# Kernel tuning notes

Measured on AMD Instinct MI355X. Metric: run time of the kernel, lower is better.

Reference implementation:

```python
import jax, jax.numpy as jnp
import numpy as np

B, W, M = 16, 32, 512
NH, HALF, K, H = 64, 32, 8, 8
LK = W // 2               # long-conv kernel size
LOUT = W - 2 * (LK - 1)   # = 2 (dilated valid conv output length)
NSP = 10                  # n_spatial (hardcoded in module)
GC1_IN = (1 + LOUT) * K   # 24


def setup_inputs() -> dict:
    key = jax.random.key(0)
    ks = jax.random.split(key, 23)
    def n(k, shp, s=0.1):
        return jax.random.normal(k, shp, jnp.float32) * s
    return dict(
        x=jax.random.normal(ks[0], (B, W, M), jnp.float32),
        adj=jax.random.uniform(ks[1], (M, M), jnp.float32) / M,  # row-normalized-ish dense adj
        Wih=n(ks[2], (NH, 1)), Whh=n(ks[3], (NH, NH)),
        bih=n(ks[4], (NH,)), bhh=n(ks[5], (NH,)),
        W1=n(ks[6], (HALF, NH)), W2=n(ks[7], (HALF, NH)), b1=n(ks[8], (HALF,)),
        V=n(ks[9], (HALF,)), bv=n(ks[10], (1,)),
        Wb=n(ks[11], (M, M)), wb=n(ks[12], (1,)),
        conv_w=n(ks[13], (K, 1, W)), conv_b=n(ks[14], (K,)),
        convl_w=n(ks[15], (K, 1, LK)), convl_b=n(ks[16], (K,)),
        gc1_w=n(ks[17], (GC1_IN, NH)), gc1_b=n(ks[18], (NH,)),
        gc2_w=n(ks[19], (NH, NSP)), gc2_b=n(ks[20], (NSP,)),
        out_w=n(ks[21], (H, NSP + NH)), out_b=n(ks[22], (H,)),
    )


def reference(x, adj, Wih, Whh, bih, bhh, W1, W2, b1, V, bv, Wb, wb,
              conv_w, conv_b, convl_w, convl_b, gc1_w, gc1_b, gc2_w, gc2_b,
              out_w, out_b):
    b = x.shape[0]
    # [b, w, m] -> per-node sequences [b*m, w]
    seq = jnp.transpose(x, (0, 2, 1)).reshape(b * M, W)

    # vanilla tanh RNN, input_size=1 (batched over all b*m series)
    inp = seq[:, :, None] * Wih[:, 0] + (bih + bhh)          # [b*m, w, nh]
    def step(h, it):
        return jnp.tanh(it + h @ Whh.T), None
    h0 = jnp.zeros((b * M, NH), x.dtype)
    last_hid, _ = jax.lax.scan(step, h0, jnp.swapaxes(inp, 0, 1))
    last_hid = last_hid.reshape(b, M, NH)                    # out_temporal

    # pairwise additive attention: a[b,i,j] = V . elu(W1 h_j + W2 h_i + b1) + bv
    e1 = last_hid @ W1.T                                     # [b, m, half] (j role)
    e2 = last_hid @ W2.T                                     # [b, m, half] (i role)
    a = jax.nn.elu(e2[:, :, None, :] + e1[:, None, :, :] + b1)  # [b,m,m,half]
    a_mx = a @ V + bv                                        # [b, m, m]
    # F.normalize(p=2, dim=1)
    norm = jnp.sqrt(jnp.sum(a_mx * a_mx, axis=1, keepdims=True))
    a_mx = a_mx / jnp.maximum(norm, 1e-12)

    # per-node short conv (kernel == window -> out len 1) as a single matmul
    r_short = seq @ conv_w[:, 0, :].T + conv_b               # [b*m, k]
    # per-node dilated long conv, batched over all b*m series
    r_long = jax.lax.conv_general_dilated(
        seq[:, None, :], convl_w, window_strides=(1,), padding='VALID',
        rhs_dilation=(2,), dimension_numbers=('NCW', 'OIW', 'NCW'))
    r_long = r_long + convl_b[None, :, None]                 # [b*m, k, LOUT]
    r = jnp.concatenate([r_short[:, :, None], r_long], axis=-1)  # [b*m, k, 1+LOUT]
    r = jax.nn.relu(r.reshape(b, M, GC1_IN))

    # gated mix of static normalized adj and learned attention adj
    c = jax.nn.sigmoid(a_mx @ Wb + wb)
    adj_mix = adj[None] * c + a_mx * (1.0 - c)               # [b, m, m]

    # two dense graph conv layers: relu(adj @ (h @ W) + b)
    h1 = jax.nn.relu(adj_mix @ (r @ gc1_w) + gc1_b)          # [b, m, nh]
    out_spatial = jax.nn.relu(adj_mix @ (h1 @ gc2_w) + gc2_b)  # [b, m, nsp]

    feat = jnp.concatenate([out_spatial, last_hid], axis=-1)  # [b, m, nsp+nh]
    out = feat @ out_w.T + out_b                              # [b, m, h]
    return jnp.transpose(out, (0, 2, 1))                      # [b, h, m]
```

## Files before the change

### kernel.cpp

```cpp
#include <hip/hip_runtime.h>


typedef __attribute__((ext_vector_type(8))) short bf16x8;
typedef __attribute__((ext_vector_type(4))) float f32x4;
#define MFMA16 __builtin_amdgcn_mfma_f32_16x16x32_bf16

__device__ __forceinline__ unsigned short f2bf(float f) {
    unsigned u = __float_as_uint(f);
    u += 0x7fff + ((u >> 16) & 1);
    return (unsigned short)(u >> 16);
}
__device__ __forceinline__ float bf2f(unsigned short h) {
    return __uint_as_float(((unsigned)h) << 16);
}
__device__ __forceinline__ float fast_tanh(float x) {
    float e = __expf(2.f * x);
    return 1.f - 2.f / (e + 1.f);
}

__global__ __launch_bounds__(256) void fused1_kernel(
    const float* __restrict__ x, const float* __restrict__ Wih,
    const float* __restrict__ Whh, const float* __restrict__ bih,
    const float* __restrict__ bhh, const float* __restrict__ W1,
    const float* __restrict__ W2, float* __restrict__ lh,
    float* __restrict__ e1, float* __restrict__ e2,
    const float* __restrict__ conv_w, const float* __restrict__ conv_b,
    const float* __restrict__ convl_w, const float* __restrict__ convl_b,
    const float* __restrict__ gc1_w, unsigned short* __restrict__ rgT,
    const float* __restrict__ Wb, unsigned short* __restrict__ WbT,
    float* __restrict__ nrmss)
{
    __shared__ __align__(16) char smem[12160];
    int blk = blockIdx.x, t = threadIdx.x;

    if (blk < 256) {
        int wid = t >> 6, lane = t & 63;
        int rowblk = blk * 32;
        int b = rowblk >> 9, mb = rowblk & 511;
        float* xs = (float*)smem;
        unsigned short* hs = (unsigned short*)(smem + 4096);
        float* rrs = (float*)(smem + 8704);

        for (int u = t; u < 1024; u += 256) {
            int tt = u >> 5, c = u & 31;
            xs[tt * 32 + c] = x[(b * 32 + tt) * 512 + mb + c];
        }
        for (int u = t; u < 2304; u += 256) hs[u] = 0;
        __syncthreads();

        if (wid < 2) {
            int l15 = lane & 15, quad = lane >> 4;
            int row0 = rowblk + wid * 16;
            unsigned short* hw0 = hs + wid * 1152;

            bf16x8 afr[4][2];
#pragma unroll
            for (int mt = 0; mt < 4; ++mt)
#pragma unroll
                for (int hf = 0; hf < 2; ++hf) {
                    const float* src = Whh + (16 * mt + l15) * 64 + 32 * hf + quad * 8;
                    union { bf16x8 v; unsigned short u[8]; } tmp;
#pragma unroll
                    for (int j = 0; j < 8; ++j) tmp.u[j] = f2bf(src[j]);
                    afr[mt][hf] = tmp.v;
                }
            bf16x8 wfr[2][2][2];
#pragma unroll
            for (int e = 0; e < 2; ++e)
#pragma unroll
                for (int nt = 0; nt < 2; ++nt)
#pragma unroll
                    for (int kf = 0; kf < 2; ++kf) {
                        const float* Wsrc = (e ? W2 : W1);
                        const float* src = Wsrc + (16 * nt + l15) * 64 + 32 * kf + quad * 8;
                        union { bf16x8 v; unsigned short u[8]; } tmp;
#pragma unroll
                        for (int j = 0; j < 8; ++j) tmp.u[j] = f2bf(src[j]);
                        wfr[e][nt][kf] = tmp.v;
                    }
            float wihv[4][4], bsv[4][4];
#pragma unroll
            for (int mt = 0; mt < 4; ++mt)
#pragma unroll
                for (int r = 0; r < 4; ++r) {
                    int n = 16 * mt + quad * 4 + r;
                    wihv[mt][r] = Wih[n];
                    bsv[mt][r]  = bih[n] + bhh[n];
                }

            float th[4][4];
            for (int tstep = 0; tstep < 32; ++tstep) {
                bf16x8 b0 = *(bf16x8*)(hw0 + l15 * 72 + quad * 8);
                bf16x8 b1 = *(bf16x8*)(hw0 + l15 * 72 + 32 + quad * 8);
                float xt = xs[tstep * 32 + wid * 16 + l15];
                f32x4 acc[4];
#pragma unroll
                for (int mt = 0; mt < 4; ++mt) {
                    f32x4 z = {0.f, 0.f, 0.f, 0.f};
                    acc[mt] = MFMA16(afr[mt][0], b0, z, 0, 0, 0);
                    acc[mt] = MFMA16(afr[mt][1], b1, acc[mt], 0, 0, 0);
                }
#pragma unroll
                for (int mt = 0; mt < 4; ++mt) {
                    ushort4 hwv;
#pragma unroll
                    for (int r = 0; r < 4; ++r)
                        th[mt][r] = fast_tanh(acc[mt][r] + xt * wihv[mt][r] + bsv[mt][r]);
                    hwv.x = f2bf(th[mt][0]); hwv.y = f2bf(th[mt][1]);
                    hwv.z = f2bf(th[mt][2]); hwv.w = f2bf(th[mt][3]);
                    *(ushort4*)(hw0 + l15 * 72 + 16 * mt + quad * 4) = hwv;
                }
            }
#pragma unroll
            for (int mt = 0; mt < 4; ++mt)
                *(float4*)(lh + (row0 + l15) * 64 + 16 * mt + quad * 4) =
                    make_float4(th[mt][0], th[mt][1], th[mt][2], th[mt][3]);

            bf16x8 a0 = *(bf16x8*)(hw0 + l15 * 72 + quad * 8);
            bf16x8 a1 = *(bf16x8*)(hw0 + l15 * 72 + 32 + quad * 8);
#pragma unroll
            for (int e = 0; e < 2; ++e) {
                float* dst = e ? e2 : e1;
#pragma unroll
                for (int nt = 0; nt < 2; ++nt) {
                    f32x4 z = {0.f, 0.f, 0.f, 0.f};
                    f32x4 ee = MFMA16(a0, wfr[e][nt][0], z, 0, 0, 0);
                    ee = MFMA16(a1, wfr[e][nt][1], ee, 0, 0, 0);
#pragma unroll
                    for (int r = 0; r < 4; ++r)
                        dst[(row0 + quad * 4 + r) * 32 + 16 * nt + l15] = ee[r];
                }
            }
        } else {
            int wid2 = wid - 2;
#pragma unroll
            for (int rep = 0; rep < 2; ++rep) {
                int task = rep * 64 + lane;
                int rl = wid2 * 16 + (task >> 3);
                int k  = task & 7;
                float s = conv_b[k];
                for (int w = 0; w < 32; ++w) s += xs[w * 32 + rl] * conv_w[k * 32 + w];
                float l0 = convl_b[k], l1 = l0;
                for (int tt = 0; tt < 16; ++tt) {
                    float wv = convl_w[k * 16 + tt];
                    l0 += xs[(2 * tt) * 32 + rl] * wv;
                    l1 += xs[(2 * tt + 1) * 32 + rl] * wv;
                }
                rrs[rl * 25 + k * 3 + 0] = fmaxf(s, 0.f);
                rrs[rl * 25 + k * 3 + 1] = fmaxf(l0, 0.f);
                rrs[rl * 25 + k * 3 + 2] = fmaxf(l1, 0.f);
            }
            __builtin_amdgcn_wave_barrier();
            int rl = wid2 * 16 + (lane & 15);
            int nb = lane >> 4;
#pragma unroll
            for (int q = 0; q < 16; ++q) {
                int n = nb * 16 + q;
                float acc = 0.f;
#pragma unroll
                for (int c = 0; c < 24; ++c) acc += rrs[rl * 25 + c] * gc1_w[c * 64 + n];
                rgT[b * 32768 + n * 512 + mb + rl] = f2bf(acc);
            }
        }
    } else if (blk < 512) {
        int bid = blk - 256;
        int nb = (bid & 15) * 32, kb = (bid >> 4) * 32;
        float* tile = (float*)smem;
        for (int u = t; u < 1024; u += 256) {
            int r = u >> 5, c = u & 31;
            tile[r * 33 + c] = Wb[(kb + r) * 512 + nb + c];
        }
        __syncthreads();
        for (int u = t; u < 1024; u += 256) {
            int r = u >> 5, c = u & 31;
            WbT[(nb + r) * 512 + kb + c] = f2bf(tile[c * 33 + r]);
        }
    } else {
        nrmss[(blk - 512) * 256 + t] = 0.f;
    }
}

__global__ __launch_bounds__(256) void amx_kernel(
    const float* __restrict__ e1, const float* __restrict__ e2,
    const float* __restrict__ b1p, const float* __restrict__ Vp,
    const float* __restrict__ bvp, unsigned short* __restrict__ amxb,
    float* __restrict__ nrmss)
{
    int bb = blockIdx.z;
    int i0 = blockIdx.y * 64, j0 = blockIdx.x * 64;
    __shared__ float e2s[64][33], e1s[64][33];
    __shared__ float Vs[32];
    __shared__ float red[16][68];
    int t = threadIdx.x;
    for (int u = t; u < 2048; u += 256) {
        int r = u >> 5, c = u & 31;
        e2s[r][c] = e2[(bb * 512 + i0 + r) * 32 + c];
        e1s[r][c] = e1[(bb * 512 + j0 + r) * 32 + c] + b1p[c];
    }
    if (t < 32) Vs[t] = Vp[t];
    __syncthreads();
    int ti = (t >> 4) * 4, tj = (t & 15) * 4;
    float acc[4][4] = {};
#pragma unroll
    for (int h = 0; h < 32; ++h) {
        float vv = Vs[h];
        float xi[4], yj[4], Exi[4], Eyj[4];
#pragma unroll
        for (int p = 0; p < 4; ++p) { xi[p] = e2s[ti + p][h]; Exi[p] = __expf(xi[p]); }
#pragma unroll
        for (int q = 0; q < 4; ++q) { yj[q] = e1s[tj + q][h]; Eyj[q] = __expf(yj[q]); }
#pragma unroll
        for (int p = 0; p < 4; ++p)
#pragma unroll
            for (int q = 0; q < 4; ++q) {
                float v = xi[p] + yj[q];
                float prod = Exi[p] * Eyj[q];
                float el = v > 0.f ? v : prod - 1.f;
                acc[p][q] += vv * el;
            }
    }
    float bv = bvp[0];
    float ss[4] = {0.f, 0.f, 0.f, 0.f};
#pragma unroll
    for (int p = 0; p < 4; ++p) {
        float v0 = acc[p][0] + bv, v1 = acc[p][1] + bv;
        float v2 = acc[p][2] + bv, v3 = acc[p][3] + bv;
        ushort4 o;
        o.x = f2bf(v0); o.y = f2bf(v1); o.z = f2bf(v2); o.w = f2bf(v3);
        *(ushort4*)(amxb + (bb * 512 + i0 + ti + p) * 512 + j0 + tj) = o;
        ss[0] += v0 * v0; ss[1] += v1 * v1; ss[2] += v2 * v2; ss[3] += v3 * v3;
    }
#pragma unroll
    for (int q = 0; q < 4; ++q) red[t >> 4][tj + q] = ss[q];
    __syncthreads();
    if (t < 64) {
        float s = 0.f;
#pragma unroll
        for (int g = 0; g < 16; ++g) s += red[g][t];
        atomicAdd(&nrmss[bb * 512 + j0 + t], s);
    }
}

__global__ __launch_bounds__(256) void gemm_adjmix(
    const unsigned short* __restrict__ amxb, const unsigned short* __restrict__ WbT,
    const float* __restrict__ wbp, const float* __restrict__ adj,
    const float* __restrict__ nrmss, unsigned short* __restrict__ adjmix)
{
    int bb = blockIdx.z;
    int i0 = blockIdx.y * 64, j0 = blockIdx.x * 64;
    __shared__ __align__(16) short As[64 * 72];
    __shared__ __align__(16) short Bs[64 * 72];
    __shared__ float rn[512];
    int t = threadIdx.x, w = t >> 6, lane = t & 63;
    int l15 = lane & 15, quad = lane >> 4;
    for (int u = t; u < 512; u += 256)
        rn[u] = 1.f / fmaxf(sqrtf(nrmss[bb * 512 + u]), 1e-12f);
    const unsigned short* Ag = amxb + bb * 262144;
    f32x4 acc[4] = {};
    for (int kk = 1; kk <= 8; ++kk) {
        int k0 = (j0 + 64 * kk) & 511;
        __syncthreads();
#pragma unroll
        for (int u0 = 0; u0 < 2; ++u0) {
            int u = t + u0 * 256;
            int i = u >> 3, o = u & 7;
            *(int4*)(Bs + i * 72 + o * 8) =
                *(const int4*)(WbT + (j0 + i) * 512 + k0 + o * 8);
            union { int4 v; unsigned short us[8]; } ur;
            ur.v = *(const int4*)(Ag + (i0 + i) * 512 + k0 + o * 8);
            union { int4 v; unsigned short us[8]; } ow;
#pragma unroll
            for (int c = 0; c < 8; ++c)
                ow.us[c] = f2bf(bf2f(ur.us[c]) * rn[k0 + o * 8 + c]);
            *(int4*)(As + i * 72 + o * 8) = ow.v;
        }
        __syncthreads();
        bf16x8 a0 = *(bf16x8*)(As + (16 * w + l15) * 72 + quad * 8);
        bf16x8 a1 = *(bf16x8*)(As + (16 * w + l15) * 72 + 32 + quad * 8);
#pragma unroll
        for (int nt = 0; nt < 4; ++nt) {
            bf16x8 b0 = *(bf16x8*)(Bs + (16 * nt + l15) * 72 + quad * 8);
            bf16x8 b1 = *(bf16x8*)(Bs + (16 * nt + l15) * 72 + 32 + quad * 8);
            acc[nt] = MFMA16(a0, b0, acc[nt], 0, 0, 0);
            acc[nt] = MFMA16(a1, b1, acc[nt], 0, 0, 0);
        }
    }
    float wb = wbp[0];
#pragma unroll
    for (int nt = 0; nt < 4; ++nt)
#pragma unroll
    for (int r = 0; r < 4; ++r) {
        int il = 16 * w + quad * 4 + r;
        int jl = 16 * nt + l15;
        int i = i0 + il, j = j0 + jl;
        float s  = acc[nt][r] + wb;
        float cv = 1.f / (1.f + __expf(-s));
        float am = bf2f((unsigned short)As[il * 72 + jl]);
        float ad = adj[i * 512 + j];
        adjmix[(bb * 512 + i) * 512 + j] = f2bf(ad * cv + am * (1.f - cv));
    }
}

__global__ __launch_bounds__(256) void gemm_h1(
    const unsigned short* __restrict__ adjmix, const unsigned short* __restrict__ rgT,
    const float* __restrict__ gc1_b, const float* __restrict__ gc2_w,
    float* __restrict__ h1g)
{
    int bb = blockIdx.y;
    int i0 = blockIdx.x * 32;
    __shared__ __align__(16) short As[32 * 72];
    __shared__ __align__(16) short Bs[64 * 72];
    __shared__ float h1s[32][72];
    int t = threadIdx.x, w = t >> 6, lane = t & 63;
    int l15 = lane & 15, quad = lane >> 4;
    int rt = w & 1, ntb = (w >> 1) * 2;
    const unsigned short* Ag = adjmix + bb * 262144;
    const unsigned short* Bg = rgT + bb * 32768;
    f32x4 acc[2] = {};
    for (int k0 = 0; k0 < 512; k0 += 64) {
        __syncthreads();
        {
            int i = t >> 3, o = t & 7;
            *(int4*)(As + i * 72 + o * 8) =
                *(const int4*)(Ag + (i0 + i) * 512 + k0 + o * 8);
        }
#pragma unroll
        for (int u0 = 0; u0 < 2; ++u0) {
            int u = t + u0 * 256;
            int i = u >> 3, o = u & 7;
            *(int4*)(Bs + i * 72 + o * 8) =
                *(const int4*)(Bg + i * 512 + k0 + o * 8);
        }
        __syncthreads();
        bf16x8 a0 = *(bf16x8*)(As + (16 * rt + l15) * 72 + quad * 8);
        bf16x8 a1 = *(bf16x8*)(As + (16 * rt + l15) * 72 + 32 + quad * 8);
#pragma unroll
        for (int q = 0; q < 2; ++q) {
            int nt = ntb + q;
            bf16x8 b0 = *(bf16x8*)(Bs + (16 * nt + l15) * 72 + quad * 8);
            bf16x8 b1 = *(bf16x8*)(Bs + (16 * nt + l15) * 72 + 32 + quad * 8);
            acc[q] = MFMA16(a0, b0, acc[q], 0, 0, 0);
            acc[q] = MFMA16(a1, b1, acc[q], 0, 0, 0);
        }
    }
#pragma unroll
    for (int q = 0; q < 2; ++q)
#pragma unroll
    for (int r = 0; r < 4; ++r) {
        int il = 16 * rt + quad * 4 + r;
        int j = 16 * (ntb + q) + l15;
        h1s[il][j] = fmaxf(acc[q][r] + gc1_b[j], 0.f);
    }
    __syncthreads();
    for (int u = t; u < 320; u += 256) {
        int row = u / 10, ns = u - row * 10;
        float a2 = 0.f;
#pragma unroll
        for (int j = 0; j < 64; ++j) a2 += h1s[row][j] * gc2_w[j * 10 + ns];
        h1g[(bb * 512 + i0 + row) * 10 + ns] = a2;
    }
}

__global__ __launch_bounds__(256) void ospout_kernel(
    const unsigned short* __restrict__ adjmix, const float* __restrict__ h1g,
    const float* __restrict__ gc2_b, const float* __restrict__ lh,
    const float* __restrict__ out_w, const float* __restrict__ out_b,
    float* __restrict__ out)
{
    int r0 = blockIdx.x * 16;
    int bb = r0 >> 9;
    int wid = threadIdx.x >> 6, lane = threadIdx.x & 63;
    __shared__ float Bsm[10][512];
    __shared__ float ow[8][80];
    __shared__ float ob[8], g2b[10];
    for (int u = threadIdx.x; u < 5120; u += 256) {
        int k = u / 10, ns = u - k * 10;
        Bsm[ns][k] = h1g[bb * 5120 + u];
    }
    if (threadIdx.x < 8)  ob[threadIdx.x]  = out_b[threadIdx.x];
    if (threadIdx.x < 10) g2b[threadIdx.x] = gc2_b[threadIdx.x];
    for (int u = threadIdx.x; u < 592; u += 256) {
        int hh = u / 74, c = u - hh * 74;
        ow[hh][c] = out_w[u];
    }
    __syncthreads();
#pragma unroll
    for (int half = 0; half < 4; ++half) {
        int row = r0 + half * 4 + wid, m = row & 511;
        const unsigned short* Ar = adjmix + row * 512;
        float a[8];
#pragma unroll
        for (int q = 0; q < 8; ++q) a[q] = bf2f(Ar[lane + 64 * q]);
        float os[10];
#pragma unroll
        for (int ns = 0; ns < 10; ++ns) {
            float s = 0.f;
#pragma unroll
            for (int q = 0; q < 8; ++q) s += a[q] * Bsm[ns][lane + 64 * q];
#pragma unroll
            for (int off = 32; off; off >>= 1) s += __shfl_xor(s, off);
            os[ns] = fmaxf(s + g2b[ns], 0.f);
        }
        float lv = lh[row * 64 + lane];
#pragma unroll
        for (int hh = 0; hh < 8; ++hh) {
            float t1 = lv * ow[hh][10 + lane];
#pragma unroll
            for (int off = 32; off; off >>= 1) t1 += __shfl_xor(t1, off);
            if (lane == hh) {
                float acc = ob[hh] + t1;
#pragma unroll
                for (int ns = 0; ns < 10; ++ns) acc += os[ns] * ow[hh][ns];
                out[bb * 4096 + hh * 512 + m] = acc;
            }
        }
    }
}

extern "C" void kernel_launch(void* const* d_in, const int* in_sizes, int n_in,
                              void* d_out, int out_size, void* d_ws, size_t ws_size,
                              hipStream_t stream)
{
    const float* x       = (const float*)d_in[0];
    const float* adj     = (const float*)d_in[1];
    const float* Wih     = (const float*)d_in[2];
    const float* Whh     = (const float*)d_in[3];
    const float* bih     = (const float*)d_in[4];
    const float* bhh     = (const float*)d_in[5];
    const float* W1      = (const float*)d_in[6];
    const float* W2      = (const float*)d_in[7];
    const float* b1      = (const float*)d_in[8];
    const float* V       = (const float*)d_in[9];
    const float* bv      = (const float*)d_in[10];
    const float* Wb      = (const float*)d_in[11];
    const float* wb      = (const float*)d_in[12];
    const float* conv_w  = (const float*)d_in[13];
    const float* conv_b  = (const float*)d_in[14];
    const float* convl_w = (const float*)d_in[15];
    const float* convl_b = (const float*)d_in[16];
    const float* gc1_w   = (const float*)d_in[17];
    const float* gc1_b   = (const float*)d_in[18];
    const float* gc2_w   = (const float*)d_in[19];
    const float* gc2_b   = (const float*)d_in[20];
    const float* out_w   = (const float*)d_in[21];
    const float* out_b   = (const float*)d_in[22];

    float* ws    = (float*)d_ws;
    float* lh    = ws;
    float* e1    = lh + 524288;
    float* e2    = e1 + 262144;
    float* nrmss = e2 + 262144;
    float* h1g   = nrmss + 8192;
    unsigned short* amxb    = (unsigned short*)(h1g + 81920);
    unsigned short* adjmixb = amxb + 4194304;
    unsigned short* WbT     = adjmixb + 4194304;
    unsigned short* rgT     = WbT + 262144;

    fused1_kernel<<<544, 256, 0, stream>>>(
        x, Wih, Whh, bih, bhh, W1, W2, lh, e1, e2,
        conv_w, conv_b, convl_w, convl_b, gc1_w, rgT, Wb, WbT, nrmss);
    amx_kernel<<<dim3(8, 8, 16), 256, 0, stream>>>(e1, e2, b1, V, bv,
                                                   amxb, nrmss);
    gemm_adjmix<<<dim3(8, 8, 16), 256, 0, stream>>>(amxb, WbT, wb, adj,
                                                    nrmss, adjmixb);
    gemm_h1<<<dim3(16, 16), 256, 0, stream>>>(adjmixb, rgT, gc1_b, gc2_w, h1g);
    ospout_kernel<<<512, 256, 0, stream>>>(adjmixb, h1g, gc2_b, lh,
                                           out_w, out_b, (float*)d_out);
}
```

Before: 207.1 us.

## Merge five kernels into one persistent kernel with global atomic barriers

Replaces the chain of five kernel launches with a single 512-block persistent kernel whose phases (RNN/conv, attention scores, adjacency-mix GEMM, first graph conv, output) are separated by a software grid barrier built on an atomic counter and spin-wait. The aim is to remove launch gaps and tail effects between stages. In exchange, the kernel relies on all 512 blocks being co-resident (launch_bounds 256,2 with enlarged shared memory), adds barrier spin overhead, and fixes the phase work into a static loop over 1024 tiles. A memset of the barrier counter is added before the launch.

```diff
diff --git a/kernel.cpp b/kernel.cpp
--- a/kernel.cpp
+++ b/kernel.cpp
@@ -18,7 +18,21 @@
     return 1.f - 2.f / (e + 1.f);
 }
 
-__global__ __launch_bounds__(256) void fused1_kernel(
+__device__ __forceinline__ void gbar(unsigned* bar, unsigned phase) {
+    __syncthreads();
+    if (threadIdx.x == 0) {
+        __threadfence();
+        atomicAdd(bar, 1u);
+        unsigned tgt = phase * 512u;
+        while (__hip_atomic_load(bar, __ATOMIC_ACQUIRE,
+                                 __HIP_MEMORY_SCOPE_AGENT) < tgt)
+            __builtin_amdgcn_s_sleep(2);
+        __threadfence();
+    }
+    __syncthreads();
+}
+
+__global__ __launch_bounds__(256, 2) void mega_kernel(
     const float* __restrict__ x, const float* __restrict__ Wih,
     const float* __restrict__ Whh, const float* __restrict__ bih,
     const float* __restrict__ bhh, const float* __restrict__ W1,
@@ -28,9 +42,18 @@
     const float* __restrict__ convl_w, const float* __restrict__ convl_b,
     const float* __restrict__ gc1_w, unsigned short* __restrict__ rgT,
     const float* __restrict__ Wb, unsigned short* __restrict__ WbT,
-    float* __restrict__ nrmss)
+    float* __restrict__ nrmss,
+    const float* __restrict__ b1p, const float* __restrict__ Vp,
+    const float* __restrict__ bvp, unsigned short* __restrict__ amxb,
+    const float* __restrict__ wbp, const float* __restrict__ adj,
+    unsigned short* __restrict__ adjmix,
+    const float* __restrict__ gc1_b, const float* __restrict__ gc2_w,
+    float* __restrict__ h1g,
+    const float* __restrict__ gc2_b,
+    const float* __restrict__ out_w, const float* __restrict__ out_b,
+    float* __restrict__ out, unsigned* __restrict__ bar)
 {
-    __shared__ __align__(16) char smem[12160];
+    __shared__ __align__(16) char smem[23296];
     int blk = blockIdx.x, t = threadIdx.x;
 
     if (blk < 256) {
@@ -162,10 +185,11 @@
                 rgT[b * 32768 + n * 512 + mb + rl] = f2bf(acc);
             }
         }
-    } else if (blk < 512) {
+    } else {
         int bid = blk - 256;
         int nb = (bid & 15) * 32, kb = (bid >> 4) * 32;
         float* tile = (float*)smem;
+        if (bid < 32) nrmss[bid * 256 + t] = 0.f;
         for (int u = t; u < 1024; u += 256) {
             int r = u >> 5, c = u & 31;
             tile[r * 33 + c] = Wb[(kb + r) * 512 + nb + c];
@@ -175,243 +199,234 @@
             int r = u >> 5, c = u & 31;
             WbT[(nb + r) * 512 + kb + c] = f2bf(tile[c * 33 + r]);
         }
-    } else {
-        nrmss[(blk - 512) * 256 + t] = 0.f;
-    }
-}
-
-__global__ __launch_bounds__(256) void amx_kernel(
-    const float* __restrict__ e1, const float* __restrict__ e2,
-    const float* __restrict__ b1p, const float* __restrict__ Vp,
-    const float* __restrict__ bvp, unsigned short* __restrict__ amxb,
-    float* __restrict__ nrmss)
-{
-    int bb = blockIdx.z;
-    int i0 = blockIdx.y * 64, j0 = blockIdx.x * 64;
-    __shared__ float e2s[64][33], e1s[64][33];
-    __shared__ float Vs[32];
-    __shared__ float red[16][68];
-    int t = threadIdx.x;
-    for (int u = t; u < 2048; u += 256) {
-        int r = u >> 5, c = u & 31;
-        e2s[r][c] = e2[(bb * 512 + i0 + r) * 32 + c];
-        e1s[r][c] = e1[(bb * 512 + j0 + r) * 32 + c] + b1p[c];
-    }
-    if (t < 32) Vs[t] = Vp[t];
-    __syncthreads();
-    int ti = (t >> 4) * 4, tj = (t & 15) * 4;
-    float acc[4][4] = {};
-#pragma unroll
-    for (int h = 0; h < 32; ++h) {
-        float vv = Vs[h];
-        float xi[4], yj[4], Exi[4], Eyj[4];
-#pragma unroll
-        for (int p = 0; p < 4; ++p) { xi[p] = e2s[ti + p][h]; Exi[p] = __expf(xi[p]); }
-#pragma unroll
-        for (int q = 0; q < 4; ++q) { yj[q] = e1s[tj + q][h]; Eyj[q] = __expf(yj[q]); }
-#pragma unroll
-        for (int p = 0; p < 4; ++p)
-#pragma unroll
-            for (int q = 0; q < 4; ++q) {
-                float v = xi[p] + yj[q];
-                float prod = Exi[p] * Eyj[q];
-                float el = v > 0.f ? v : prod - 1.f;
-                acc[p][q] += vv * el;
-            }
-    }
-    float bv = bvp[0];
-    float ss[4] = {0.f, 0.f, 0.f, 0.f};
-#pragma unroll
-    for (int p = 0; p < 4; ++p) {
-        float v0 = acc[p][0] + bv, v1 = acc[p][1] + bv;
-        float v2 = acc[p][2] + bv, v3 = acc[p][3] + bv;
-        ushort4 o;
-        o.x = f2bf(v0); o.y = f2bf(v1); o.z = f2bf(v2); o.w = f2bf(v3);
-        *(ushort4*)(amxb + (bb * 512 + i0 + ti + p) * 512 + j0 + tj) = o;
-        ss[0] += v0 * v0; ss[1] += v1 * v1; ss[2] += v2 * v2; ss[3] += v3 * v3;
-    }
-#pragma unroll
-    for (int q = 0; q < 4; ++q) red[t >> 4][tj + q] = ss[q];
-    __syncthreads();
-    if (t < 64) {
-        float s = 0.f;
-#pragma unroll
-        for (int g = 0; g < 16; ++g) s += red[g][t];
-        atomicAdd(&nrmss[bb * 512 + j0 + t], s);
-    }
-}
-
-__global__ __launch_bounds__(256) void gemm_adjmix(
-    const unsigned short* __restrict__ amxb, const unsigned short* __restrict__ WbT,
-    const float* __restrict__ wbp, const float* __restrict__ adj,
-    const float* __restrict__ nrmss, unsigned short* __restrict__ adjmix)
-{
-    int bb = blockIdx.z;
-    int i0 = blockIdx.y * 64, j0 = blockIdx.x * 64;
-    __shared__ __align__(16) short As[64 * 72];
-    __shared__ __align__(16) short Bs[64 * 72];
-    __shared__ float rn[512];
-    int t = threadIdx.x, w = t >> 6, lane = t & 63;
-    int l15 = lane & 15, quad = lane >> 4;
-    for (int u = t; u < 512; u += 256)
-        rn[u] = 1.f / fmaxf(sqrtf(nrmss[bb * 512 + u]), 1e-12f);
-    const unsigned short* Ag = amxb + bb * 262144;
-    f32x4 acc[4] = {};
-    for (int kk = 1; kk <= 8; ++kk) {
-        int k0 = (j0 + 64 * kk) & 511;
-        __syncthreads();
-#pragma unroll
-        for (int u0 = 0; u0 < 2; ++u0) {
-            int u = t + u0 * 256;
-            int i = u >> 3, o = u & 7;
-            *(int4*)(Bs + i * 72 + o * 8) =
-                *(const int4*)(WbT + (j0 + i) * 512 + k0 + o * 8);
-            union { int4 v; unsigned short us[8]; } ur;
-            ur.v = *(const int4*)(Ag + (i0 + i) * 512 + k0 + o * 8);
-            union { int4 v; unsigned short us[8]; } ow;
-#pragma unroll
-            for (int c = 0; c < 8; ++c)
-                ow.us[c] = f2bf(bf2f(ur.us[c]) * rn[k0 + o * 8 + c]);
-            *(int4*)(As + i * 72 + o * 8) = ow.v;
-        }
-        __syncthreads();
-        bf16x8 a0 = *(bf16x8*)(As + (16 * w + l15) * 72 + quad * 8);
-        bf16x8 a1 = *(bf16x8*)(As + (16 * w + l15) * 72 + 32 + quad * 8);
-#pragma unroll
-        for (int nt = 0; nt < 4; ++nt) {
-            bf16x8 b0 = *(bf16x8*)(Bs + (16 * nt + l15) * 72 + quad * 8);
-            bf16x8 b1 = *(bf16x8*)(Bs + (16 * nt + l15) * 72 + 32 + quad * 8);
-            acc[nt] = MFMA16(a0, b0, acc[nt], 0, 0, 0);
-            acc[nt] = MFMA16(a1, b1, acc[nt], 0, 0, 0);
-        }
-    }
-    float wb = wbp[0];
-#pragma unroll
-    for (int nt = 0; nt < 4; ++nt)
-#pragma unroll
-    for (int r = 0; r < 4; ++r) {
-        int il = 16 * w + quad * 4 + r;
-        int jl = 16 * nt + l15;
-        int i = i0 + il, j = j0 + jl;
-        float s  = acc[nt][r] + wb;
-        float cv = 1.f / (1.f + __expf(-s));
-        float am = bf2f((unsigned short)As[il * 72 + jl]);
-        float ad = adj[i * 512 + j];
-        adjmix[(bb * 512 + i) * 512 + j] = f2bf(ad * cv + am * (1.f - cv));
-    }
-}
-
-__global__ __launch_bounds__(256) void gemm_h1(
-    const unsigned short* __restrict__ adjmix, const unsigned short* __restrict__ rgT,
-    const float* __restrict__ gc1_b, const float* __restrict__ gc2_w,
-    float* __restrict__ h1g)
-{
-    int bb = blockIdx.y;
-    int i0 = blockIdx.x * 32;
-    __shared__ __align__(16) short As[32 * 72];
-    __shared__ __align__(16) short Bs[64 * 72];
-    __shared__ float h1s[32][72];
-    int t = threadIdx.x, w = t >> 6, lane = t & 63;
-    int l15 = lane & 15, quad = lane >> 4;
-    int rt = w & 1, ntb = (w >> 1) * 2;
-    const unsigned short* Ag = adjmix + bb * 262144;
-    const unsigned short* Bg = rgT + bb * 32768;
-    f32x4 acc[2] = {};
-    for (int k0 = 0; k0 < 512; k0 += 64) {
-        __syncthreads();
-        {
-            int i = t >> 3, o = t & 7;
-            *(int4*)(As + i * 72 + o * 8) =
-                *(const int4*)(Ag + (i0 + i) * 512 + k0 + o * 8);
-        }
-#pragma unroll
-        for (int u0 = 0; u0 < 2; ++u0) {
-            int u = t + u0 * 256;
-            int i = u >> 3, o = u & 7;
-            *(int4*)(Bs + i * 72 + o * 8) =
-                *(const int4*)(Bg + i * 512 + k0 + o * 8);
-        }
-        __syncthreads();
-        bf16x8 a0 = *(bf16x8*)(As + (16 * rt + l15) * 72 + quad * 8);
-        bf16x8 a1 = *(bf16x8*)(As + (16 * rt + l15) * 72 + 32 + quad * 8);
-#pragma unroll
-        for (int q = 0; q < 2; ++q) {
-            int nt = ntb + q;
-            bf16x8 b0 = *(bf16x8*)(Bs + (16 * nt + l15) * 72 + quad * 8);
-            bf16x8 b1 = *(bf16x8*)(Bs + (16 * nt + l15) * 72 + 32 + quad * 8);
-            acc[q] = MFMA16(a0, b0, acc[q], 0, 0, 0);
-            acc[q] = MFMA16(a1, b1, acc[q], 0, 0, 0);
-        }
-    }
-#pragma unroll
-    for (int q = 0; q < 2; ++q)
-#pragma unroll
-    for (int r = 0; r < 4; ++r) {
-        int il = 16 * rt + quad * 4 + r;
-        int j = 16 * (ntb + q) + l15;
-        h1s[il][j] = fmaxf(acc[q][r] + gc1_b[j], 0.f);
-    }
-    __syncthreads();
-    for (int u = t; u < 320; u += 256) {
-        int row = u / 10, ns = u - row * 10;
-        float a2 = 0.f;
-#pragma unroll
-        for (int j = 0; j < 64; ++j) a2 += h1s[row][j] * gc2_w[j * 10 + ns];
-        h1g[(bb * 512 + i0 + row) * 10 + ns] = a2;
-    }
-}
-
-__global__ __launch_bounds__(256) void ospout_kernel(
-    const unsigned short* __restrict__ adjmix, const float* __restrict__ h1g,
-    const float* __restrict__ gc2_b, const float* __restrict__ lh,
-    const float* __restrict__ out_w, const float* __restrict__ out_b,
-    float* __restrict__ out)
-{
-    int r0 = blockIdx.x * 16;
-    int bb = r0 >> 9;
-    int wid = threadIdx.x >> 6, lane = threadIdx.x & 63;
-    __shared__ float Bsm[10][512];
-    __shared__ float ow[8][80];
-    __shared__ float ob[8], g2b[10];
-    for (int u = threadIdx.x; u < 5120; u += 256) {
-        int k = u / 10, ns = u - k * 10;
-        Bsm[ns][k] = h1g[bb * 5120 + u];
-    }
-    if (threadIdx.x < 8)  ob[threadIdx.x]  = out_b[threadIdx.x];
-    if (threadIdx.x < 10) g2b[threadIdx.x] = gc2_b[threadIdx.x];
-    for (int u = threadIdx.x; u < 592; u += 256) {
-        int hh = u / 74, c = u - hh * 74;
-        ow[hh][c] = out_w[u];
-    }
-    __syncthreads();
-#pragma unroll
-    for (int half = 0; half < 4; ++half) {
-        int row = r0 + half * 4 + wid, m = row & 511;
-        const unsigned short* Ar = adjmix + row * 512;
-        float a[8];
-#pragma unroll
-        for (int q = 0; q < 8; ++q) a[q] = bf2f(Ar[lane + 64 * q]);
-        float os[10];
-#pragma unroll
-        for (int ns = 0; ns < 10; ++ns) {
+    }
+
+    gbar(bar, 1);
+
+    for (int tid = blk; tid < 1024; tid += 512) {
+        __syncthreads();
+        int bb = tid >> 6;
+        int i0 = ((tid >> 3) & 7) * 64, j0 = (tid & 7) * 64;
+        float* e2s = (float*)smem;
+        float* e1s = (float*)(smem + 8448);
+        float* Vs  = (float*)(smem + 16896);
+        float* red = (float*)(smem + 17024);
+        for (int u = t; u < 2048; u += 256) {
+            int r = u >> 5, c = u & 31;
+            e2s[r * 33 + c] = e2[(bb * 512 + i0 + r) * 32 + c];
+            e1s[r * 33 + c] = e1[(bb * 512 + j0 + r) * 32 + c] + b1p[c];
+        }
+        if (t < 32) Vs[t] = Vp[t];
+        __syncthreads();
+        int ti = (t >> 4) * 4, tj = (t & 15) * 4;
+        float acc[4][4] = {};
+#pragma unroll
+        for (int h = 0; h < 32; ++h) {
+            float vv = Vs[h];
+            float xi[4], yj[4], Exi[4], Eyj[4];
+#pragma unroll
+            for (int p = 0; p < 4; ++p) { xi[p] = e2s[(ti + p) * 33 + h]; Exi[p] = __expf(xi[p]); }
+#pragma unroll
+            for (int q = 0; q < 4; ++q) { yj[q] = e1s[(tj + q) * 33 + h]; Eyj[q] = __expf(yj[q]); }
+#pragma unroll
+            for (int p = 0; p < 4; ++p)
+#pragma unroll
+                for (int q = 0; q < 4; ++q) {
+                    float v = xi[p] + yj[q];
+                    float prod = Exi[p] * Eyj[q];
+                    float el = v > 0.f ? v : prod - 1.f;
+                    acc[p][q] += vv * el;
+                }
+        }
+        float bv = bvp[0];
+        float ss[4] = {0.f, 0.f, 0.f, 0.f};
+#pragma unroll
+        for (int p = 0; p < 4; ++p) {
+            float v0 = acc[p][0] + bv, v1 = acc[p][1] + bv;
+            float v2 = acc[p][2] + bv, v3 = acc[p][3] + bv;
+            ushort4 o;
+            o.x = f2bf(v0); o.y = f2bf(v1); o.z = f2bf(v2); o.w = f2bf(v3);
+            *(ushort4*)(amxb + (bb * 512 + i0 + ti + p) * 512 + j0 + tj) = o;
+            ss[0] += v0 * v0; ss[1] += v1 * v1; ss[2] += v2 * v2; ss[3] += v3 * v3;
+        }
+#pragma unroll
+        for (int q = 0; q < 4; ++q) red[(t >> 4) * 68 + tj + q] = ss[q];
+        __syncthreads();
+        if (t < 64) {
             float s = 0.f;
 #pragma unroll
-            for (int q = 0; q < 8; ++q) s += a[q] * Bsm[ns][lane + 64 * q];
-#pragma unroll
-            for (int off = 32; off; off >>= 1) s += __shfl_xor(s, off);
-            os[ns] = fmaxf(s + g2b[ns], 0.f);
-        }
-        float lv = lh[row * 64 + lane];
-#pragma unroll
-        for (int hh = 0; hh < 8; ++hh) {
-            float t1 = lv * ow[hh][10 + lane];
-#pragma unroll
-            for (int off = 32; off; off >>= 1) t1 += __shfl_xor(t1, off);
-            if (lane == hh) {
-                float acc = ob[hh] + t1;
-#pragma unroll
-                for (int ns = 0; ns < 10; ++ns) acc += os[ns] * ow[hh][ns];
-                out[bb * 4096 + hh * 512 + m] = acc;
+            for (int g = 0; g < 16; ++g) s += red[g * 68 + t];
+            atomicAdd(&nrmss[bb * 512 + j0 + t], s);
+        }
+    }
+
+    gbar(bar, 2);
+
+    for (int tid = blk; tid < 1024; tid += 512) {
+        __syncthreads();
+        int bb = tid >> 6;
+        int i0 = ((tid >> 3) & 7) * 64, j0 = (tid & 7) * 64;
+        short* As = (short*)smem;
+        short* Bs = (short*)(smem + 9216);
+        float* rn = (float*)(smem + 18432);
+        int w = t >> 6, lane = t & 63;
+        int l15 = lane & 15, quad = lane >> 4;
+        for (int u = t; u < 512; u += 256)
+            rn[u] = 1.f / fmaxf(sqrtf(nrmss[bb * 512 + u]), 1e-12f);
+        const unsigned short* Ag = amxb + bb * 262144;
+        f32x4 acc[4] = {};
+        for (int kk = 1; kk <= 8; ++kk) {
+            int k0 = (j0 + 64 * kk) & 511;
+            __syncthreads();
+#pragma unroll
+            for (int u0 = 0; u0 < 2; ++u0) {
+                int u = t + u0 * 256;
+                int i = u >> 3, o = u & 7;
+                *(int4*)(Bs + i * 72 + o * 8) =
+                    *(const int4*)(WbT + (j0 + i) * 512 + k0 + o * 8);
+                union { int4 v; unsigned short us[8]; } ur;
+                ur.v = *(const int4*)(Ag + (i0 + i) * 512 + k0 + o * 8);
+                union { int4 v; unsigned short us[8]; } ow;
+#pragma unroll
+                for (int c = 0; c < 8; ++c)
+                    ow.us[c] = f2bf(bf2f(ur.us[c]) * rn[k0 + o * 8 + c]);
+                *(int4*)(As + i * 72 + o * 8) = ow.v;
+            }
+            __syncthreads();
+            bf16x8 a0 = *(bf16x8*)(As + (16 * w + l15) * 72 + quad * 8);
+            bf16x8 a1 = *(bf16x8*)(As + (16 * w + l15) * 72 + 32 + quad * 8);
+#pragma unroll
+            for (int nt = 0; nt < 4; ++nt) {
+                bf16x8 b0 = *(bf16x8*)(Bs + (16 * nt + l15) * 72 + quad * 8);
+                bf16x8 b1 = *(bf16x8*)(Bs + (16 * nt + l15) * 72 + 32 + quad * 8);
+                acc[nt] = MFMA16(a0, b0, acc[nt], 0, 0, 0);
+                acc[nt] = MFMA16(a1, b1, acc[nt], 0, 0, 0);
+            }
+        }
+        float wb = wbp[0];
+#pragma unroll
+        for (int nt = 0; nt < 4; ++nt)
+#pragma unroll
+        for (int r = 0; r < 4; ++r) {
+            int il = 16 * w + quad * 4 + r;
+            int jl = 16 * nt + l15;
+            int i = i0 + il, j = j0 + jl;
+            float s  = acc[nt][r] + wb;
+            float cv = 1.f / (1.f + __expf(-s));
+            float am = bf2f((unsigned short)As[il * 72 + jl]);
+            float ad = adj[i * 512 + j];
+            adjmix[(bb * 512 + i) * 512 + j] = f2bf(ad * cv + am * (1.f - cv));
+        }
+    }
+
+    gbar(bar, 3);
+
+    if (blk < 256) {
+        int bb = blk >> 4;
+        int i0 = (blk & 15) * 32;
+        short* As  = (short*)smem;
+        short* Bs  = (short*)(smem + 4608);
+        float* h1s = (float*)(smem + 13824);
+        int w = t >> 6, lane = t & 63;
+        int l15 = lane & 15, quad = lane >> 4;
+        int rt = w & 1, ntb = (w >> 1) * 2;
+        const unsigned short* Ag = adjmix + bb * 262144;
+        const unsigned short* Bg = rgT + bb * 32768;
+        f32x4 acc[2] = {};
+        for (int k0 = 0; k0 < 512; k0 += 64) {
+            __syncthreads();
+            {
+                int i = t >> 3, o = t & 7;
+                *(int4*)(As + i * 72 + o * 8) =
+                    *(const int4*)(Ag + (i0 + i) * 512 + k0 + o * 8);
+            }
+#pragma unroll
+            for (int u0 = 0; u0 < 2; ++u0) {
+                int u = t + u0 * 256;
+                int i = u >> 3, o = u & 7;
+                *(int4*)(Bs + i * 72 + o * 8) =
+                    *(const int4*)(Bg + i * 512 + k0 + o * 8);
+            }
+            __syncthreads();
+            bf16x8 a0 = *(bf16x8*)(As + (16 * rt + l15) * 72 + quad * 8);
+            bf16x8 a1 = *(bf16x8*)(As + (16 * rt + l15) * 72 + 32 + quad * 8);
+#pragma unroll
+            for (int q = 0; q < 2; ++q) {
+                int nt = ntb + q;
+                bf16x8 b0 = *(bf16x8*)(Bs + (16 * nt + l15) * 72 + quad * 8);
+                bf16x8 b1 = *(bf16x8*)(Bs + (16 * nt + l15) * 72 + 32 + quad * 8);
+                acc[q] = MFMA16(a0, b0, acc[q], 0, 0, 0);
+                acc[q] = MFMA16(a1, b1, acc[q], 0, 0, 0);
+            }
+        }
+#pragma unroll
+        for (int q = 0; q < 2; ++q)
+#pragma unroll
+        for (int r = 0; r < 4; ++r) {
+            int il = 16 * rt + quad * 4 + r;
+            int j = 16 * (ntb + q) + l15;
+            h1s[il * 72 + j] = fmaxf(acc[q][r] + gc1_b[j], 0.f);
+        }
+        __syncthreads();
+        for (int u = t; u < 320; u += 256) {
+            int row = u / 10, ns = u - row * 10;
+            float a2 = 0.f;
+#pragma unroll
+            for (int j = 0; j < 64; ++j) a2 += h1s[row * 72 + j] * gc2_w[j * 10 + ns];
+            h1g[(bb * 512 + i0 + row) * 10 + ns] = a2;
+        }
+    }
+
+    gbar(bar, 4);
+
+    {
+        int r0 = blk * 16;
+        int bb = r0 >> 9;
+        int wid = t >> 6, lane = t & 63;
+        float* Bsm = (float*)smem;
+        float* ow  = (float*)(smem + 20480);
+        float* ob  = (float*)(smem + 23040);
+        float* g2b = (float*)(smem + 23072);
+        for (int u = t; u < 5120; u += 256) {
+            int k = u / 10, ns = u - k * 10;
+            Bsm[ns * 512 + k] = h1g[bb * 5120 + u];
+        }
+        if (t < 8)  ob[t]  = out_b[t];
+        if (t < 10) g2b[t] = gc2_b[t];
+        for (int u = t; u < 592; u += 256) {
+            int hh = u / 74, c = u - hh * 74;
+            ow[hh * 80 + c] = out_w[u];
+        }
+        __syncthreads();
+#pragma unroll
+        for (int half = 0; half < 4; ++half) {
+            int row = r0 + half * 4 + wid, m = row & 511;
+            const unsigned short* Ar = adjmix + row * 512;
+            float a[8];
+#pragma unroll
+            for (int q = 0; q < 8; ++q) a[q] = bf2f(Ar[lane + 64 * q]);
+            float os[10];
+#pragma unroll
+            for (int ns = 0; ns < 10; ++ns) {
+                float s = 0.f;
+#pragma unroll
+                for (int q = 0; q < 8; ++q) s += a[q] * Bsm[ns * 512 + lane + 64 * q];
+#pragma unroll
+                for (int off = 32; off; off >>= 1) s += __shfl_xor(s, off);
+                os[ns] = fmaxf(s + g2b[ns], 0.f);
+            }
+            float lv = lh[row * 64 + lane];
+#pragma unroll
+            for (int hh = 0; hh < 8; ++hh) {
+                float t1 = lv * ow[hh * 80 + 10 + lane];
+#pragma unroll
+                for (int off = 32; off; off >>= 1) t1 += __shfl_xor(t1, off);
+                if (lane == hh) {
+                    float acc = ob[hh] + t1;
+#pragma unroll
+                    for (int ns = 0; ns < 10; ++ns) acc += os[ns] * ow[hh * 80 + ns];
+                    out[bb * 4096 + hh * 512 + m] = acc;
+                }
             }
         }
     }
@@ -455,15 +470,12 @@
     unsigned short* adjmixb = amxb + 4194304;
     unsigned short* WbT     = adjmixb + 4194304;
     unsigned short* rgT     = WbT + 262144;
-
-    fused1_kernel<<<544, 256, 0, stream>>>(
+    unsigned* bar = (unsigned*)(rgT + 524288);
+
+    hipMemsetAsync(bar, 0, 64, stream);
+    mega_kernel<<<512, 256, 0, stream>>>(
         x, Wih, Whh, bih, bhh, W1, W2, lh, e1, e2,
-        conv_w, conv_b, convl_w, convl_b, gc1_w, rgT, Wb, WbT, nrmss);
-    amx_kernel<<<dim3(8, 8, 16), 256, 0, stream>>>(e1, e2, b1, V, bv,
-                                                   amxb, nrmss);
-    gemm_adjmix<<<dim3(8, 8, 16), 256, 0, stream>>>(amxb, WbT, wb, adj,
-                                                    nrmss, adjmixb);
-    gemm_h1<<<dim3(16, 16), 256, 0, stream>>>(adjmixb, rgT, gc1_b, gc2_w, h1g);
-    ospout_kernel<<<512, 256, 0, stream>>>(adjmixb, h1g, gc2_b, lh,
-                                           out_w, out_b, (float*)d_out);
-}
+        conv_w, conv_b, convl_w, convl_b, gc1_w, rgT, Wb, WbT, nrmss,
+        b1, V, bv, amxb, wb, adj, adjmixb,
+        gc1_b, gc2_w, h1g, gc2_b, out_w, out_b, (float*)d_out, bar);
+}
```

Result: slower. 463.3 us (+123.7%).
